# Kernel tuning notes

Measured on AMD Instinct MI355X. Metric: run time of the kernel, lower is better.

The kernel has to match this reference:

```python
import jax, jax.numpy as jnp
import numpy as np

N_NODES = 100000
N_EDGES = 625000
DIM = 128

def setup_inputs() -> dict:
    key = jax.random.key(0)
    k1, k2, k3, k4 = jax.random.split(key, 4)
    scale = 1.0 / np.sqrt(DIM)
    x = jax.random.normal(k1, (N_NODES, DIM), dtype=jnp.float32)
    edge_index = jax.random.randint(k2, (2, N_EDGES), 0, N_NODES, dtype=jnp.int64)
    W_l = jax.random.normal(k3, (DIM, DIM), dtype=jnp.float32) * scale
    W_r = jax.random.normal(k4, (DIM, DIM), dtype=jnp.float32) * scale
    b = jnp.zeros((DIM,), dtype=jnp.float32)
    return {"x": x, "edge_index": edge_index, "W_l": W_l, "W_r": W_r, "b": b}

def reference(x, edge_index, W_l, W_r, b):
    # PyG SAGEConv (mean aggr): out_i = W_l @ mean_{j in N(i)} x_j + W_r @ x_i + b
    n = x.shape[0]
    src = edge_index[0]  # message sources
    dst = edge_index[1]  # message targets
    msgs = x[src]                                             # [E, D] gather
    agg = jax.ops.segment_sum(msgs, dst, num_segments=n)      # [N, D] scatter-add
    cnt = jax.ops.segment_sum(jnp.ones((src.shape[0],), dtype=x.dtype), dst, num_segments=n)
    mean = agg / jnp.maximum(cnt, 1.0)[:, None]               # mean aggregation
    out = mean @ W_l.T + x @ W_r.T + b                        # neighbor + root transform
    out = jax.nn.relu(out)
    # dropout in eval mode = identity; original returns (x, edge_attr=None)
    return out
```

## Files before the change

kernel.cpp:

```cpp
#include <hip/hip_runtime.h>

#define NNODES 100000
#define NEDGES 625000
#define DIM 128
#define NTILES 782
#define ZBLK 98
#define BCAP 64

typedef short short8 __attribute__((ext_vector_type(8)));
typedef unsigned short ushort8 __attribute__((ext_vector_type(8)));
typedef float f32x4  __attribute__((ext_vector_type(4)));

__device__ __forceinline__ unsigned short f2bf(float f) {
    unsigned u = __float_as_uint(f);
    u += 0x7FFFu + ((u >> 16) & 1u);
    return (unsigned short)(u >> 16);
}
__device__ __forceinline__ float bf_lo(unsigned u) { return __uint_as_float(u << 16); }
__device__ __forceinline__ float bf_hi(unsigned u) { return __uint_as_float(u & 0xFFFF0000u); }

template<bool ZBF>
__global__ __launch_bounds__(512, 6) void gemm_zero_kernel(
    const float* __restrict__ x,
    const float* __restrict__ Wl,
    const float* __restrict__ Wr,
    unsigned short* __restrict__ Yh,
    unsigned short* __restrict__ Zh,
    float* __restrict__ Z,
    int* __restrict__ cnt)
{
    __shared__ unsigned short wfrag[16384];
    const int tid = threadIdx.x;

    if (blockIdx.x >= NTILES) {
        int i = (blockIdx.x - NTILES) * 1024 + tid * 2;
        if (i < NNODES) {
            if (i + 1 < NNODES) *(int2*)(cnt + i) = (int2){0, 0};
            else cnt[i] = 0;
        }
        return;
    }

    const int wave = tid >> 6;
    const int lane = tid & 63;
    const int lrow = lane & 15;
    const int kgrp = lane >> 4;
    const int row0 = blockIdx.x * 128 + wave * 16;

    int arow = row0 + lrow;
    if (arow >= NNODES) arow = NNODES - 1;
    const float* xrow = x + (size_t)arow * DIM + kgrp * 8;
    short8 af[4];
#pragma unroll
    for (int ks = 0; ks < 4; ++ks) {
        float4 a0 = *(const float4*)(xrow + ks * 32);
        float4 a1 = *(const float4*)(xrow + ks * 32 + 4);
        af[ks][0] = (short)f2bf(a0.x); af[ks][1] = (short)f2bf(a0.y);
        af[ks][2] = (short)f2bf(a0.z); af[ks][3] = (short)f2bf(a0.w);
        af[ks][4] = (short)f2bf(a1.x); af[ks][5] = (short)f2bf(a1.y);
        af[ks][6] = (short)f2bf(a1.z); af[ks][7] = (short)f2bf(a1.w);
    }

#pragma unroll
    for (int it = 0; it < 4; ++it) {
        const int i  = it * 512 + tid;
        const int il = i & 63;
        const int ks = (i >> 6) & 3;
        const int ct = i >> 8;
        const float* wr = Wl + (size_t)(ct * 16 + (il & 15)) * DIM
                             + (ks * 4 + (il >> 4)) * 8;
        float4 w0 = *(const float4*)(wr);
        float4 w1 = *(const float4*)(wr + 4);
        ushort8 c;
        c[0] = f2bf(w0.x); c[1] = f2bf(w0.y); c[2] = f2bf(w0.z); c[3] = f2bf(w0.w);
        c[4] = f2bf(w1.x); c[5] = f2bf(w1.y); c[6] = f2bf(w1.z); c[7] = f2bf(w1.w);
        *(ushort8*)(wfrag + (size_t)i * 8) = c;
    }
    __syncthreads();

    {
        f32x4 acc[8];
#pragma unroll
        for (int i = 0; i < 8; ++i) acc[i] = (f32x4){0.f, 0.f, 0.f, 0.f};
#pragma unroll
        for (int ks = 0; ks < 4; ++ks)
#pragma unroll
            for (int ct = 0; ct < 8; ++ct) {
                short8 bf = *(const short8*)(wfrag + (size_t)((ct * 4 + ks) * 64 + lane) * 8);
                acc[ct] = __builtin_amdgcn_mfma_f32_16x16x32_bf16(af[ks], bf, acc[ct], 0, 0, 0);
            }
#pragma unroll
        for (int r = 0; r < 4; ++r) {
            const int row = row0 + kgrp * 4 + r;
            if (row < NNODES) {
                ushort8 y;
#pragma unroll
                for (int ct = 0; ct < 8; ++ct) y[ct] = f2bf(acc[ct][r]);
                *(ushort8*)(Yh + (size_t)row * DIM + lrow * 8) = y;
            }
        }
    }

    __syncthreads();

#pragma unroll
    for (int it = 0; it < 4; ++it) {
        const int i  = it * 512 + tid;
        const int il = i & 63;
        const int ks = (i >> 6) & 3;
        const int ct = i >> 8;
        const float* wr = Wr + (size_t)(ct * 16 + (il & 15)) * DIM
                             + (ks * 4 + (il >> 4)) * 8;
        float4 w0 = *(const float4*)(wr);
        float4 w1 = *(const float4*)(wr + 4);
        ushort8 c;
        c[0] = f2bf(w0.x); c[1] = f2bf(w0.y); c[2] = f2bf(w0.z); c[3] = f2bf(w0.w);
        c[4] = f2bf(w1.x); c[5] = f2bf(w1.y); c[6] = f2bf(w1.z); c[7] = f2bf(w1.w);
        *(ushort8*)(wfrag + (size_t)i * 8) = c;
    }
    __syncthreads();

    {
        f32x4 acc[8];
#pragma unroll
        for (int i = 0; i < 8; ++i) acc[i] = (f32x4){0.f, 0.f, 0.f, 0.f};
#pragma unroll
        for (int ks = 0; ks < 4; ++ks)
#pragma unroll
            for (int ct = 0; ct < 8; ++ct) {
                short8 bf = *(const short8*)(wfrag + (size_t)((ct * 4 + ks) * 64 + lane) * 8);
                acc[ct] = __builtin_amdgcn_mfma_f32_16x16x32_bf16(af[ks], bf, acc[ct], 0, 0, 0);
            }
#pragma unroll
        for (int r = 0; r < 4; ++r) {
            const int row = row0 + kgrp * 4 + r;
            if (row < NNODES) {
                if (ZBF) {
                    ushort8 zz;
#pragma unroll
                    for (int ct = 0; ct < 8; ++ct) zz[ct] = f2bf(acc[ct][r]);
                    *(ushort8*)(Zh + (size_t)row * DIM + lrow * 8) = zz;
                } else {
                    float4 z0, z1;
                    z0.x = acc[0][r]; z0.y = acc[1][r]; z0.z = acc[2][r]; z0.w = acc[3][r];
                    z1.x = acc[4][r]; z1.y = acc[5][r]; z1.z = acc[6][r]; z1.w = acc[7][r];
                    *(float4*)(Z + (size_t)row * DIM + lrow * 8)     = z0;
                    *(float4*)(Z + (size_t)row * DIM + lrow * 8 + 4) = z1;
                }
            }
        }
    }
}

__global__ void fill_kernel(const int* __restrict__ ei,
                            int* __restrict__ cnt, int* __restrict__ adjb) {
    int e = blockIdx.x * 256 + threadIdx.x;
    if (e >= NEDGES) return;
    int src = ei[e];
    int dst = ei[NEDGES + e];
    int p = atomicAdd(&cnt[dst], 1);
    if (p < BCAP) adjb[(size_t)dst * BCAP + p] = src;
}

template<bool ZBF>
__global__ __launch_bounds__(256) void aggregate_kernel(
    const unsigned short* __restrict__ Yh,
    const unsigned short* __restrict__ Zh,
    const int* __restrict__ cnt,
    const int* __restrict__ adjb,
    const float* __restrict__ bias,
    float* __restrict__ out)
{
    const int tid = threadIdx.x;
    const int l16 = tid & 15;
    const int n = blockIdx.x * 16 + (tid >> 4);
    if (n >= NNODES) return;

    int deg = cnt[n];
    if (deg > BCAP) deg = BCAP;

    float bb[8], z[8];
#pragma unroll
    for (int m = 0; m < 8; ++m) bb[m] = bias[16 * m + l16];
    if (ZBF) {
        uint4 zv = *(const uint4*)(Zh + (size_t)n * DIM + l16 * 8);
        z[0] = bf_lo(zv.x); z[1] = bf_hi(zv.x); z[2] = bf_lo(zv.y); z[3] = bf_hi(zv.y);
        z[4] = bf_lo(zv.z); z[5] = bf_hi(zv.z); z[6] = bf_lo(zv.w); z[7] = bf_hi(zv.w);
    } else {
        float4 z0 = *(const float4*)(out + (size_t)n * DIM + l16 * 8);
        float4 z1 = *(const float4*)(out + (size_t)n * DIM + l16 * 8 + 4);
        z[0] = z0.x; z[1] = z0.y; z[2] = z0.z; z[3] = z0.w;
        z[4] = z1.x; z[5] = z1.y; z[6] = z1.z; z[7] = z1.w;
    }

    float a[8];
#pragma unroll
    for (int m = 0; m < 8; ++m) a[m] = 0.f;

    const int* bkt = adjb + (size_t)n * BCAP;
    for (int j = 0; j < deg; j += 8) {
        const int rem = deg - j;
        int s[8];
#pragma unroll
        for (int k = 0; k < 8; ++k) {
            int idx = j + k;
            s[k] = bkt[(idx < deg) ? idx : (deg - 1)];
        }
        uint4 v[8];
#pragma unroll
        for (int k = 0; k < 8; ++k)
            v[k] = *(const uint4*)(Yh + (size_t)s[k] * DIM + l16 * 8);
#pragma unroll
        for (int k = 0; k < 8; ++k) {
            if (k < rem) {
                a[0] += bf_lo(v[k].x); a[1] += bf_hi(v[k].x);
                a[2] += bf_lo(v[k].y); a[3] += bf_hi(v[k].y);
                a[4] += bf_lo(v[k].z); a[5] += bf_hi(v[k].z);
                a[6] += bf_lo(v[k].w); a[7] += bf_hi(v[k].w);
            }
        }
    }

    const float invd = 1.0f / fmaxf((float)deg, 1.0f);
#pragma unroll
    for (int m = 0; m < 8; ++m)
        out[(size_t)n * DIM + 16 * m + l16] = fmaxf(a[m] * invd + z[m] + bb[m], 0.f);
}

extern "C" void kernel_launch(void* const* d_in, const int* in_sizes, int n_in,
                              void* d_out, int out_size, void* d_ws, size_t ws_size,
                              hipStream_t stream) {
    const float* x  = (const float*)d_in[0];
    const int*   ei = (const int*)d_in[1];
    const float* Wl = (const float*)d_in[2];
    const float* Wr = (const float*)d_in[3];
    const float* b  = (const float*)d_in[4];
    float* out = (float*)d_out;

    int*            cnt  = (int*)d_ws;
    int*            adjb = (int*)((char*)d_ws + (1ull << 20));
    unsigned short* Yh   = (unsigned short*)((char*)d_ws + (27ull << 20));
    unsigned short* Zh   = (unsigned short*)((char*)d_ws + (53ull << 20));

    const size_t need_zbf = (53ull << 20) + (size_t)NNODES * DIM * 2;
    const bool zbf = (ws_size >= need_zbf);

    if (zbf) {
        gemm_zero_kernel<true><<<NTILES + ZBLK, 512, 0, stream>>>(x, Wl, Wr, Yh, Zh, out, cnt);
        fill_kernel<<<(NEDGES + 255) / 256, 256, 0, stream>>>(ei, cnt, adjb);
        aggregate_kernel<true><<<(NNODES + 15) / 16, 256, 0, stream>>>(Yh, Zh, cnt, adjb, b, out);
    } else {
        gemm_zero_kernel<false><<<NTILES + ZBLK, 512, 0, stream>>>(x, Wl, Wr, Yh, Zh, out, cnt);
        fill_kernel<<<(NEDGES + 255) / 256, 256, 0, stream>>>(ei, cnt, adjb);
        aggregate_kernel<false><<<(NNODES + 15) / 16, 256, 0, stream>>>(Yh, Zh, cnt, adjb, b, out);
    }
}
```

Baseline: 100.1 us.

## Fuse edge-fill into GEMM kernel and zero counts with memset

Edge bucketing (atomic count and adjacency fill) now runs in extra blocks of the GEMM kernel instead of its own launch. The zeroing of the count array moves to a hipMemsetAsync issued before that kernel, because the fill blocks need zeroed counters before they start. The aim is to overlap the memory- and atomic-bound fill work with the compute-bound GEMM tiles and to save one kernel launch. Launch bounds drop from 6 to 4 blocks per SM. Fill blocks also now carry 512 threads and the GEMM's LDS allocation, which may reduce how many fit at once.

```diff
diff --git a/kernel.cpp b/kernel.cpp
--- a/kernel.cpp
+++ b/kernel.cpp
@@ -4,7 +4,7 @@
 #define NEDGES 625000
 #define DIM 128
 #define NTILES 782
-#define ZBLK 98
+#define FBLK 1221
 #define BCAP 64
 
 typedef short short8 __attribute__((ext_vector_type(8)));
@@ -20,23 +20,28 @@
 __device__ __forceinline__ float bf_hi(unsigned u) { return __uint_as_float(u & 0xFFFF0000u); }
 
 template<bool ZBF>
-__global__ __launch_bounds__(512, 6) void gemm_zero_kernel(
+__global__ __launch_bounds__(512, 4) void gemm_fill_kernel(
     const float* __restrict__ x,
     const float* __restrict__ Wl,
     const float* __restrict__ Wr,
     unsigned short* __restrict__ Yh,
     unsigned short* __restrict__ Zh,
     float* __restrict__ Z,
-    int* __restrict__ cnt)
+    const int* __restrict__ ei,
+    int* __restrict__ cnt,
+    int* __restrict__ adjb)
 {
     __shared__ unsigned short wfrag[16384];
     const int tid = threadIdx.x;
-
-    if (blockIdx.x >= NTILES) {
-        int i = (blockIdx.x - NTILES) * 1024 + tid * 2;
-        if (i < NNODES) {
-            if (i + 1 < NNODES) *(int2*)(cnt + i) = (int2){0, 0};
-            else cnt[i] = 0;
+    const int bid = blockIdx.x;
+
+    if (bid >= NTILES) {
+        int e = (bid - NTILES) * 512 + tid;
+        if (e < NEDGES) {
+            int src = ei[e];
+            int dst = ei[NEDGES + e];
+            int p = atomicAdd(&cnt[dst], 1);
+            if (p < BCAP) adjb[(size_t)dst * BCAP + p] = src;
         }
         return;
     }
@@ -45,7 +50,7 @@
     const int lane = tid & 63;
     const int lrow = lane & 15;
     const int kgrp = lane >> 4;
-    const int row0 = blockIdx.x * 128 + wave * 16;
+    const int row0 = bid * 128 + wave * 16;
 
     int arow = row0 + lrow;
     if (arow >= NNODES) arow = NNODES - 1;
@@ -152,16 +157,6 @@
     }
 }
 
-__global__ void fill_kernel(const int* __restrict__ ei,
-                            int* __restrict__ cnt, int* __restrict__ adjb) {
-    int e = blockIdx.x * 256 + threadIdx.x;
-    if (e >= NEDGES) return;
-    int src = ei[e];
-    int dst = ei[NEDGES + e];
-    int p = atomicAdd(&cnt[dst], 1);
-    if (p < BCAP) adjb[(size_t)dst * BCAP + p] = src;
-}
-
 template<bool ZBF>
 __global__ __launch_bounds__(256) void aggregate_kernel(
     const unsigned short* __restrict__ Yh,
@@ -245,13 +240,13 @@
     const size_t need_zbf = (53ull << 20) + (size_t)NNODES * DIM * 2;
     const bool zbf = (ws_size >= need_zbf);
 
+    hipMemsetAsync(cnt, 0, NNODES * sizeof(int), stream);
+
     if (zbf) {
-        gemm_zero_kernel<true><<<NTILES + ZBLK, 512, 0, stream>>>(x, Wl, Wr, Yh, Zh, out, cnt);
-        fill_kernel<<<(NEDGES + 255) / 256, 256, 0, stream>>>(ei, cnt, adjb);
+        gemm_fill_kernel<true><<<NTILES + FBLK, 512, 0, stream>>>(x, Wl, Wr, Yh, Zh, out, ei, cnt, adjb);
         aggregate_kernel<true><<<(NNODES + 15) / 16, 256, 0, stream>>>(Yh, Zh, cnt, adjb, b, out);
     } else {
-        gemm_zero_kernel<false><<<NTILES + ZBLK, 512, 0, stream>>>(x, Wl, Wr, Yh, Zh, out, cnt);
-        fill_kernel<<<(NEDGES + 255) / 256, 256, 0, stream>>>(ei, cnt, adjb);
+        gemm_fill_kernel<false><<<NTILES + FBLK, 512, 0, stream>>>(x, Wl, Wr, Yh, Zh, out, ei, cnt, adjb);
         aggregate_kernel<false><<<(NNODES + 15) / 16, 256, 0, stream>>>(Yh, Zh, cnt, adjb, b, out);
     }
 }
```

Result: slower. 117.6 us (+17.5%).
